# Optimization experiments

Measured on AMD Instinct MI355X. Metric: run time of the kernel, lower is better.

## Reference

```python
import jax, jax.numpy as jnp
import numpy as np

S = 4096  # source_sequence_size
Q = 4096  # query_sequence_size
E = 2048  # embedding_size
D = 2048  # output_embedding_size


def setup_inputs() -> dict:
    key = jax.random.key(0)
    ks = jax.random.split(key, 9)
    s = 1.0 / np.sqrt(E)
    return {
        "key": jax.random.normal(ks[0], (S, E), jnp.float32),
        "value": jax.random.normal(ks[1], (S, E), jnp.float32),
        "query": jax.random.normal(ks[2], (Q, E), jnp.float32),
        "Wk": jax.random.normal(ks[3], (D, E), jnp.float32) * s,
        "bk": jax.random.normal(ks[4], (D,), jnp.float32) * 0.01,
        "Wq": jax.random.normal(ks[5], (D, E), jnp.float32) * s,
        "bq": jax.random.normal(ks[6], (D,), jnp.float32) * 0.01,
        "Wv": jax.random.normal(ks[7], (D, E), jnp.float32) * s,
        "bv": jax.random.normal(ks[8], (D,), jnp.float32) * 0.01,
    }


def reference(key, value, query, Wk, bk, Wq, bq, Wv, bv):
    # Linear projections (nn.Linear: x @ W.T + b)
    k = key @ Wk.T + bk      # [S, D]
    v = value @ Wv.T + bv    # [S, D]
    q = query @ Wq.T + bq    # [Q, D]
    # Per-query-token attention scores over all source tokens (schema BOTH),
    # then weighted sum over value rows -- vectorized form of the per-token
    # apply_attention_scores loop.
    scale = 1.0 / jnp.sqrt(jnp.asarray(D, q.dtype))
    scores = jax.nn.softmax(jnp.einsum("qd,sd->qs", q, k) * scale, axis=-1)  # [Q, S]
    return jnp.einsum("qs,sd->qd", scores, v)  # [Q, D]
```

## Files before the change

kernel.cpp:

```cpp
#include <hip/hip_runtime.h>

#define S_SEQ 4096
#define Q_SEQ 4096
#define E_DIM 2048
#define D_DIM 2048

typedef __bf16 bf16;
typedef __bf16 bf16x4 __attribute__((ext_vector_type(4)));
typedef __bf16 bf16x8 __attribute__((ext_vector_type(8)));
typedef float f32x4 __attribute__((ext_vector_type(4)));

__global__ __launch_bounds__(256) void cast6(
    const float* __restrict__ i0, const float* __restrict__ i1,
    const float* __restrict__ i2, const float* __restrict__ i3,
    const float* __restrict__ i4, const float* __restrict__ i5,
    bf16* __restrict__ o0, bf16* __restrict__ o1, bf16* __restrict__ o2,
    bf16* __restrict__ o3, bf16* __restrict__ o4, bf16* __restrict__ o5) {
  const float* in;
  bf16* out;
  int n4;
  switch (blockIdx.y) {
    case 0: in = i0; out = o0; n4 = (S_SEQ * E_DIM) / 4; break;
    case 1: in = i1; out = o1; n4 = (S_SEQ * E_DIM) / 4; break;
    case 2: in = i2; out = o2; n4 = (S_SEQ * E_DIM) / 4; break;
    case 3: in = i3; out = o3; n4 = (D_DIM * E_DIM) / 4; break;
    case 4: in = i4; out = o4; n4 = (D_DIM * E_DIM) / 4; break;
    default: in = i5; out = o5; n4 = (D_DIM * E_DIM) / 4; break;
  }
  int i = blockIdx.x * 256 + threadIdx.x;
  if (i < n4) {
    float4 v = reinterpret_cast<const float4*>(in)[i];
    bf16x4 o;
    o[0] = (bf16)v.x; o[1] = (bf16)v.y; o[2] = (bf16)v.z; o[3] = (bf16)v.w;
    *reinterpret_cast<bf16x4*>(out + 4 * (size_t)i) = o;
  }
}

__device__ __forceinline__ void async_copy16(const bf16* g, bf16* l) {
  __builtin_amdgcn_global_load_lds(
      (const __attribute__((address_space(1))) void*)g,
      (__attribute__((address_space(3))) void*)l, 16, 0, 0);
}

__device__ __forceinline__ void xcd_remap32(int id, int nt, int& m, int& n) {
  int xcd = id & 7;
  int lid = id >> 3;
  m = (xcd & 3) * 8 + (lid & 7);
  n = (xcd >> 2) * (nt >> 1) + (lid >> 3);
}
__device__ __forceinline__ void xcd_remap16(int id, int nt, int& m, int& n) {
  int xcd = id & 7;
  int lid = id >> 3;
  m = (xcd & 3) * 4 + (lid & 3);
  n = (xcd >> 2) * (nt >> 1) + (lid >> 2);
}

template <int EPI>
__device__ __forceinline__ void gemm_body_sb(
    const bf16* __restrict__ A, int lda,
    const bf16* __restrict__ B, int ldb,
    void* __restrict__ C, int ldc,
    const float* __restrict__ aux, float scale, int K, int mBase, int nBase) {
  __shared__ __align__(16) bf16 Als[128 * 64];
  __shared__ __align__(16) bf16 Bls[128 * 64];

  const int tid  = threadIdx.x;
  const int wave = tid >> 6;
  const int lane = tid & 63;
  const int quad = lane >> 4;
  const int lrow = lane & 15;
  const int wRow = (wave >> 1) * 64;
  const int wCol = (wave & 1) * 64;

  f32x4 acc[4][4];
#pragma unroll
  for (int i = 0; i < 4; ++i)
#pragma unroll
    for (int j = 0; j < 4; ++j) {
      f32x4 z = {0.f, 0.f, 0.f, 0.f};
      acc[i][j] = z;
    }

  for (int k0 = 0; k0 < K; k0 += 64) {
#pragma unroll
    for (int c = 0; c < 4; ++c) {
      int chunk = c * 256 + tid;
      int row = chunk >> 3;
      int kc = (chunk & 7) ^ (row & 7);
      const bf16* g = A + (size_t)(mBase + row) * lda + k0 + kc * 8;
      async_copy16(g, Als + (size_t)(c * 256 + wave * 64) * 8);
    }
#pragma unroll
    for (int c = 0; c < 4; ++c) {
      int chunk = c * 256 + tid;
      int row = chunk >> 3;
      int kc = (chunk & 7) ^ (row & 7);
      const bf16* g = B + (size_t)(nBase + row) * ldb + k0 + kc * 8;
      async_copy16(g, Bls + (size_t)(c * 256 + wave * 64) * 8);
    }
    __syncthreads();

#pragma unroll
    for (int kk = 0; kk < 2; ++kk) {
      bf16x8 af[4], bfr[4];
#pragma unroll
      for (int i = 0; i < 4; ++i) {
        int r = wRow + i * 16 + lrow;
        int slot = (kk * 4 + quad) ^ (r & 7);
        af[i] = *(const bf16x8*)(Als + (size_t)r * 64 + slot * 8);
      }
#pragma unroll
      for (int j = 0; j < 4; ++j) {
        int r = wCol + j * 16 + lrow;
        int slot = (kk * 4 + quad) ^ (r & 7);
        bfr[j] = *(const bf16x8*)(Bls + (size_t)r * 64 + slot * 8);
      }
#pragma unroll
      for (int i = 0; i < 4; ++i)
#pragma unroll
        for (int j = 0; j < 4; ++j)
          acc[i][j] = __builtin_amdgcn_mfma_f32_16x16x32_bf16(af[i], bfr[j], acc[i][j], 0, 0, 0);
    }
    __syncthreads();
  }

  float rinv[4][4];
  if (EPI == 2) {
#pragma unroll
    for (int i = 0; i < 4; ++i)
#pragma unroll
      for (int r = 0; r < 4; ++r)
        rinv[i][r] = aux[mBase + wRow + i * 16 + quad * 4 + r];
  }
#pragma unroll
  for (int j = 0; j < 4; ++j) {
    const int cn = nBase + wCol + j * 16 + lrow;
    float bj = 0.f;
    if (EPI == 0) bj = aux[cn];
#pragma unroll
    for (int i = 0; i < 4; ++i) {
      const int rbase = mBase + wRow + i * 16 + quad * 4;
#pragma unroll
      for (int r = 0; r < 4; ++r) {
        if (EPI == 0)
          ((bf16*)C)[(size_t)(rbase + r) * ldc + cn] = (bf16)(acc[i][j][r] + bj);
        else if (EPI == 1)
          ((bf16*)C)[(size_t)(rbase + r) * ldc + cn] =
              (bf16)__expf(acc[i][j][r] * scale);
        else
          ((float*)C)[(size_t)(rbase + r) * ldc + cn] = acc[i][j][r] * rinv[i][r];
      }
    }
  }
}

__device__ __forceinline__ void stage_half(const bf16* __restrict__ G, int ld,
                                           int grow0, int k0, bf16* lds,
                                           int wave, int lane) {
#pragma unroll
  for (int s = 0; s < 2; ++s) {
    int c = (wave * 2 + s) * 64 + lane;
    int row = c >> 3;
    int kc = (c & 7) ^ (row & 7);
    const bf16* g = G + (size_t)(grow0 + row) * ld + k0 + kc * 8;
    async_copy16(g, lds + (size_t)(wave * 2 + s) * 512);
  }
}

#define BARRIER __builtin_amdgcn_s_barrier()
#define LGKM0 asm volatile("s_waitcnt lgkmcnt(0)" ::: "memory")
#define VMCNT2 asm volatile("s_waitcnt vmcnt(2)" ::: "memory")
#define VMCNT0 asm volatile("s_waitcnt vmcnt(0)" ::: "memory")

#define RD_A(buf, IP)                                                         \
  _Pragma("unroll") for (int ii = 0; ii < 2; ++ii)                            \
  _Pragma("unroll") for (int kk = 0; kk < 2; ++kk)                            \
      aR[ii][kk] = *(const bf16x8*)(&Als[buf][(size_t)(wRow + ((IP)*2 + ii) * 16 + lrow) * 64 + slotk[kk] * 8]);

#define RD_B(buf, JP, dst)                                                    \
  _Pragma("unroll") for (int jj = 0; jj < 2; ++jj)                            \
  _Pragma("unroll") for (int kk = 0; kk < 2; ++kk)                            \
      dst[jj][kk] = *(const bf16x8*)(&Bls[buf][(size_t)(wCol + ((JP)*2 + jj) * 16 + lrow) * 64 + slotk[kk] * 8]);

#define MMA16(IP)                                                              \
  __builtin_amdgcn_s_setprio(1);                                               \
  _Pragma("unroll") for (int jj = 0; jj < 2; ++jj)                             \
  _Pragma("unroll") for (int ii = 0; ii < 2; ++ii)                             \
  _Pragma("unroll") for (int kk = 0; kk < 2; ++kk)                             \
      acc[(IP)*2 + ii][jj] = __builtin_amdgcn_mfma_f32_16x16x32_bf16(          \
          aR[ii][kk], b0[jj][kk], acc[(IP)*2 + ii][jj], 0, 0, 0);              \
  _Pragma("unroll") for (int jj = 0; jj < 2; ++jj)                             \
  _Pragma("unroll") for (int ii = 0; ii < 2; ++ii)                             \
  _Pragma("unroll") for (int kk = 0; kk < 2; ++kk)                             \
      acc[(IP)*2 + ii][2 + jj] = __builtin_amdgcn_mfma_f32_16x16x32_bf16(      \
          aR[ii][kk], b1[jj][kk], acc[(IP)*2 + ii][2 + jj], 0, 0, 0);          \
  __builtin_amdgcn_s_setprio(0)

template <int EPI>
__device__ __forceinline__ void gemm_body_4ph(
    const bf16* __restrict__ A, int lda,
    const bf16* __restrict__ B, int ldb,
    void* __restrict__ C, int ldc,
    const float* __restrict__ aux, float scale, int K, int mBase, int nBase) {
  __shared__ __align__(16) bf16 Als[2][256 * 64];
  __shared__ __align__(16) bf16 Bls[2][128 * 64];

  const int tid  = threadIdx.x;
  const int wave = tid >> 6;
  const int lane = tid & 63;
  const int quad = lane >> 4;
  const int lrow = lane & 15;
  const int wRow = (wave >> 1) * 64;
  const int wCol = (wave & 1) * 64;
  const int slotk[2] = {quad ^ (lrow & 7), (4 + quad) ^ (lrow & 7)};

  f32x4 acc[4][4];
#pragma unroll
  for (int i = 0; i < 4; ++i)
#pragma unroll
    for (int j = 0; j < 4; ++j) {
      f32x4 z = {0.f, 0.f, 0.f, 0.f};
      acc[i][j] = z;
    }

  bf16x8 aR[2][2], b0[2][2], b1[2][2];

  stage_half(B, ldb, nBase, 0, &Bls[0][0], wave, lane);
  stage_half(A, lda, mBase, 0, &Als[0][0], wave, lane);
  stage_half(A, lda, mBase + 128, 0, &Als[0][128 * 64], wave, lane);
  stage_half(B, ldb, nBase, 64, &Bls[1][0], wave, lane);
  VMCNT2;
  BARRIER;

  const int NI = K >> 7;
#pragma unroll 1
  for (int i = 0; i < NI; ++i) {
    const bool nl = (i + 1 < NI);
    const int kb = i * 128;
    RD_A(0, 0);
    RD_B(0, 0, b0);
    RD_B(0, 1, b1);
    stage_half(A, lda, mBase, kb + 64, &Als[1][0], wave, lane);
    stage_half(A, lda, mBase + 128, kb + 64, &Als[1][128 * 64], wave, lane);
    BARRIER; LGKM0; MMA16(0); BARRIER;
    RD_A(0, 1);
    if (nl) {
      stage_half(B, ldb, nBase, kb + 128, &Bls[0][0], wave, lane);
      VMCNT2;
    } else {
      VMCNT0;
    }
    BARRIER; LGKM0; MMA16(1); BARRIER;
    RD_A(1, 0);
    RD_B(1, 0, b0);
    RD_B(1, 1, b1);
    if (nl) {
      stage_half(A, lda, mBase, kb + 128, &Als[0][0], wave, lane);
      stage_half(A, lda, mBase + 128, kb + 128, &Als[0][128 * 64], wave, lane);
    }
    BARRIER; LGKM0; MMA16(0); BARRIER;
    RD_A(1, 1);
    if (nl) {
      stage_half(B, ldb, nBase, kb + 192, &Bls[1][0], wave, lane);
      VMCNT2;
    }
    BARRIER; LGKM0; MMA16(1); BARRIER;
  }

  float rinv[4][4];
  if (EPI == 2) {
#pragma unroll
    for (int i = 0; i < 4; ++i)
#pragma unroll
      for (int r = 0; r < 4; ++r)
        rinv[i][r] = aux[mBase + wRow + i * 16 + quad * 4 + r];
  }
#pragma unroll
  for (int j = 0; j < 4; ++j) {
    const int cn = nBase + wCol + j * 16 + lrow;
    float bj = 0.f;
    if (EPI == 0) bj = aux[cn];
#pragma unroll
    for (int i = 0; i < 4; ++i) {
      const int rbase = mBase + wRow + i * 16 + quad * 4;
#pragma unroll
      for (int r = 0; r < 4; ++r) {
        if (EPI == 0)
          ((bf16*)C)[(size_t)(rbase + r) * ldc + cn] = (bf16)(acc[i][j][r] + bj);
        else if (EPI == 1)
          ((bf16*)C)[(size_t)(rbase + r) * ldc + cn] =
              (bf16)__expf(acc[i][j][r] * scale);
        else
          ((float*)C)[(size_t)(rbase + r) * ldc + cn] = acc[i][j][r] * rinv[i][r];
      }
    }
  }
}

__global__ __launch_bounds__(512, 2) void qk_gemm(
    const bf16* __restrict__ A, const bf16* __restrict__ B,
    bf16* __restrict__ E, float scale) {
  int m, n;
  xcd_remap16(blockIdx.x, 32, m, n);
  gemm_body_4ph<1>(A, D_DIM, B, D_DIM, (void*)E, S_SEQ, nullptr, scale, D_DIM,
                   m * 256, n * 128);
}

__global__ __launch_bounds__(512, 2) void pv_gemm(
    const bf16* __restrict__ E, const bf16* __restrict__ vT,
    float* __restrict__ out, const float* __restrict__ inv) {
  int m, n;
  xcd_remap16(blockIdx.x, 16, m, n);
  gemm_body_4ph<2>(E, S_SEQ, vT, S_SEQ, (void*)out, D_DIM, inv, 0.f, S_SEQ,
                   m * 256, n * 128);
}

__global__ __launch_bounds__(256, 2) void proj_gemm(
    const bf16* __restrict__ xk, const bf16* __restrict__ xq,
    const bf16* __restrict__ xv,
    const bf16* __restrict__ Wk, const bf16* __restrict__ Wq,
    const bf16* __restrict__ Wv,
    const float* __restrict__ bk, const float* __restrict__ bq,
    const float* __restrict__ bv,
    bf16* __restrict__ ok, bf16* __restrict__ oq, bf16* __restrict__ ov) {
  const bf16 *A, *W;
  const float* b;
  bf16* o;
  switch (blockIdx.z) {
    case 0: A = xk; W = Wk; b = bk; o = ok; break;
    case 1: A = xq; W = Wq; b = bq; o = oq; break;
    default: A = xv; W = Wv; b = bv; o = ov; break;
  }
  int m, n;
  xcd_remap32(blockIdx.x, 16, m, n);
  gemm_body_sb<0>(A, E_DIM, W, E_DIM, (void*)o, D_DIM, b, 0.f, E_DIM,
                  m * 128, n * 128);
}

__global__ __launch_bounds__(256) void transpose_bf16(
    const bf16* __restrict__ in, bf16* __restrict__ out) {
  __shared__ bf16 tile[64][66];
  const int t = threadIdx.x;
  const int c0 = blockIdx.x * 64;
  const int r0 = blockIdx.y * 64;
  const int col = t & 63;
  const int r4 = t >> 6;
#pragma unroll
  for (int i = 0; i < 16; ++i) {
    int rr = i * 4 + r4;
    tile[rr][col] = in[(size_t)(r0 + rr) * D_DIM + c0 + col];
  }
  __syncthreads();
#pragma unroll
  for (int i = 0; i < 16; ++i) {
    int rr = i * 4 + r4;
    out[(size_t)(c0 + rr) * S_SEQ + r0 + col] = tile[col][rr];
  }
}

__global__ __launch_bounds__(256) void rowsum_inv(
    const bf16* __restrict__ E, float* __restrict__ inv) {
  const int t = threadIdx.x;
  const int wave = t >> 6;
  const int lane = t & 63;
  const int row = blockIdx.x * 4 + wave;
  const bf16x8* src = (const bf16x8*)(E + (size_t)row * S_SEQ);
  float s = 0.f;
#pragma unroll
  for (int i = 0; i < 8; ++i) {
    bf16x8 v = src[lane + i * 64];
#pragma unroll
    for (int j = 0; j < 8; ++j) s += (float)v[j];
  }
#pragma unroll
  for (int off = 32; off > 0; off >>= 1)
    s += __shfl_down(s, off, 64);
  if (lane == 0) inv[row] = 1.0f / s;
}

extern "C" void kernel_launch(void* const* d_in, const int* in_sizes, int n_in,
                              void* d_out, int out_size, void* d_ws, size_t ws_size,
                              hipStream_t stream) {
  const float* key   = (const float*)d_in[0];
  const float* value = (const float*)d_in[1];
  const float* query = (const float*)d_in[2];
  const float* Wk = (const float*)d_in[3];
  const float* bk = (const float*)d_in[4];
  const float* Wq = (const float*)d_in[5];
  const float* bq = (const float*)d_in[6];
  const float* Wv = (const float*)d_in[7];
  const float* bv = (const float*)d_in[8];

  const size_t MB = 1ull << 20;
  char* ws = (char*)d_ws;
  bf16* key_bf   = (bf16*)(ws + 0 * MB);
  bf16* value_bf = (bf16*)(ws + 16 * MB);
  bf16* query_bf = (bf16*)(ws + 32 * MB);
  bf16* Wk_bf    = (bf16*)(ws + 48 * MB);
  bf16* Wq_bf    = (bf16*)(ws + 56 * MB);
  bf16* Wv_bf    = (bf16*)(ws + 64 * MB);
  bf16* k_bf     = (bf16*)(ws + 72 * MB);
  bf16* q_bf     = (bf16*)(ws + 88 * MB);
  bf16* v_bf     = (bf16*)(ws + 104 * MB);
  bf16* vT_bf    = (bf16*)(ws + 120 * MB);
  bf16* E        = (bf16*)(ws + 0 * MB);
  float* inv     = (float*)(ws + 34 * MB);

  dim3 blk(256);
  dim3 blk512(512);

  cast6<<<dim3(8192, 6), blk, 0, stream>>>(
      key, value, query, Wk, Wq, Wv,
      key_bf, value_bf, query_bf, Wk_bf, Wq_bf, Wv_bf);

  proj_gemm<<<dim3(512, 1, 3), blk, 0, stream>>>(
      key_bf, query_bf, value_bf, Wk_bf, Wq_bf, Wv_bf, bk, bq, bv,
      k_bf, q_bf, v_bf);

  transpose_bf16<<<dim3(D_DIM / 64, S_SEQ / 64), blk, 0, stream>>>(v_bf, vT_bf);

  const float scale = 0.022097086912079608f;
  qk_gemm<<<dim3(512), blk512, 0, stream>>>(q_bf, k_bf, E, scale);

  rowsum_inv<<<dim3(1024), blk, 0, stream>>>(E, inv);

  pv_gemm<<<dim3(256), blk512, 0, stream>>>(E, vT_bf, (float*)d_out, inv);
}
```

Before: 416.0 us.

## Fuse softmax row-sum into QK epilogue and fold V transpose into QK launch

The QK GEMM epilogue now sums the bf16 exponentials it writes, reduces them across lanes, and stores per-64-column partial row sums. A tiny kernel then adds 64 partials per row to get the inverse normaliser, replacing a pass that re-read the whole 4096x4096 score matrix. The V transpose moves into extra blocks appended to the QK grid, removing one launch and letting it overlap the GEMM. The cost is extra epilogue shuffles in the QK kernel, and transpose blocks that reserve the GEMM's shared-memory footprint.

```diff
diff --git a/kernel.cpp b/kernel.cpp
--- a/kernel.cpp
+++ b/kernel.cpp
@@ -201,7 +201,8 @@
     const bf16* __restrict__ A, int lda,
     const bf16* __restrict__ B, int ldb,
     void* __restrict__ C, int ldc,
-    const float* __restrict__ aux, float scale, int K, int mBase, int nBase) {
+    const float* __restrict__ aux, float scale, int K, int mBase, int nBase,
+    float* __restrict__ psum) {
   __shared__ __align__(16) bf16 Als[2][256 * 64];
   __shared__ __align__(16) bf16 Bls[2][128 * 64];
 
@@ -275,6 +276,13 @@
       for (int r = 0; r < 4; ++r)
         rinv[i][r] = aux[mBase + wRow + i * 16 + quad * 4 + r];
   }
+  float sp[4][4];
+  if (EPI == 1) {
+#pragma unroll
+    for (int i = 0; i < 4; ++i)
+#pragma unroll
+      for (int r = 0; r < 4; ++r) sp[i][r] = 0.f;
+  }
 #pragma unroll
   for (int j = 0; j < 4; ++j) {
     const int cn = nBase + wCol + j * 16 + lrow;
@@ -285,13 +293,35 @@
       const int rbase = mBase + wRow + i * 16 + quad * 4;
 #pragma unroll
       for (int r = 0; r < 4; ++r) {
-        if (EPI == 0)
+        if (EPI == 0) {
           ((bf16*)C)[(size_t)(rbase + r) * ldc + cn] = (bf16)(acc[i][j][r] + bj);
-        else if (EPI == 1)
-          ((bf16*)C)[(size_t)(rbase + r) * ldc + cn] =
-              (bf16)__expf(acc[i][j][r] * scale);
-        else
+        } else if (EPI == 1) {
+          bf16 eb = (bf16)__expf(acc[i][j][r] * scale);
+          ((bf16*)C)[(size_t)(rbase + r) * ldc + cn] = eb;
+          sp[i][r] += (float)eb;
+        } else {
           ((float*)C)[(size_t)(rbase + r) * ldc + cn] = acc[i][j][r] * rinv[i][r];
+        }
+      }
+    }
+  }
+  if (EPI == 1) {
+#pragma unroll
+    for (int i = 0; i < 4; ++i)
+#pragma unroll
+      for (int r = 0; r < 4; ++r) {
+#pragma unroll
+        for (int off = 1; off < 16; off <<= 1)
+          sp[i][r] += __shfl_xor(sp[i][r], off, 64);
+      }
+    if (lrow == 0) {
+      const int col64 = (nBase + wCol) >> 6;
+#pragma unroll
+      for (int i = 0; i < 4; ++i) {
+        const int rbase = mBase + wRow + i * 16 + quad * 4;
+#pragma unroll
+        for (int r = 0; r < 4; ++r)
+          psum[(size_t)(rbase + r) * 64 + col64] = sp[i][r];
       }
     }
   }
@@ -299,11 +329,39 @@
 
 __global__ __launch_bounds__(512, 2) void qk_gemm(
     const bf16* __restrict__ A, const bf16* __restrict__ B,
-    bf16* __restrict__ E, float scale) {
+    bf16* __restrict__ E, float scale,
+    const bf16* __restrict__ v, bf16* __restrict__ vT,
+    float* __restrict__ psum) {
+  if (blockIdx.x >= 512) {
+    __shared__ bf16 ttile[64][66];
+    const int t = threadIdx.x;
+    const int col = t & 63;
+    const int r8 = t >> 6;
+    const int base = (blockIdx.x - 512) * 4;
+#pragma unroll 1
+    for (int t4 = 0; t4 < 4; ++t4) {
+      const int id = base + t4;
+      const int c0 = (id & 31) * 64;
+      const int r0 = (id >> 5) * 64;
+#pragma unroll
+      for (int i = 0; i < 8; ++i) {
+        int rr = i * 8 + r8;
+        ttile[rr][col] = v[(size_t)(r0 + rr) * D_DIM + c0 + col];
+      }
+      __syncthreads();
+#pragma unroll
+      for (int i = 0; i < 8; ++i) {
+        int rr = i * 8 + r8;
+        vT[(size_t)(c0 + rr) * S_SEQ + r0 + col] = ttile[col][rr];
+      }
+      __syncthreads();
+    }
+    return;
+  }
   int m, n;
   xcd_remap16(blockIdx.x, 32, m, n);
   gemm_body_4ph<1>(A, D_DIM, B, D_DIM, (void*)E, S_SEQ, nullptr, scale, D_DIM,
-                   m * 256, n * 128);
+                   m * 256, n * 128, psum);
 }
 
 __global__ __launch_bounds__(512, 2) void pv_gemm(
@@ -312,7 +370,7 @@
   int m, n;
   xcd_remap16(blockIdx.x, 16, m, n);
   gemm_body_4ph<2>(E, S_SEQ, vT, S_SEQ, (void*)out, D_DIM, inv, 0.f, S_SEQ,
-                   m * 256, n * 128);
+                   m * 256, n * 128, nullptr);
 }
 
 __global__ __launch_bounds__(256, 2) void proj_gemm(
@@ -337,45 +395,17 @@
                   m * 128, n * 128);
 }
 
-__global__ __launch_bounds__(256) void transpose_bf16(
-    const bf16* __restrict__ in, bf16* __restrict__ out) {
-  __shared__ bf16 tile[64][66];
-  const int t = threadIdx.x;
-  const int c0 = blockIdx.x * 64;
-  const int r0 = blockIdx.y * 64;
-  const int col = t & 63;
-  const int r4 = t >> 6;
+__global__ __launch_bounds__(256) void rowsum2(
+    const float* __restrict__ psum, float* __restrict__ inv) {
+  const int r = blockIdx.x * 256 + threadIdx.x;
+  const f32x4* p = (const f32x4*)(psum + (size_t)r * 64);
+  float s = 0.f;
 #pragma unroll
   for (int i = 0; i < 16; ++i) {
-    int rr = i * 4 + r4;
-    tile[rr][col] = in[(size_t)(r0 + rr) * D_DIM + c0 + col];
-  }
-  __syncthreads();
-#pragma unroll
-  for (int i = 0; i < 16; ++i) {
-    int rr = i * 4 + r4;
-    out[(size_t)(c0 + rr) * S_SEQ + r0 + col] = tile[col][rr];
-  }
-}
-
-__global__ __launch_bounds__(256) void rowsum_inv(
-    const bf16* __restrict__ E, float* __restrict__ inv) {
-  const int t = threadIdx.x;
-  const int wave = t >> 6;
-  const int lane = t & 63;
-  const int row = blockIdx.x * 4 + wave;
-  const bf16x8* src = (const bf16x8*)(E + (size_t)row * S_SEQ);
-  float s = 0.f;
-#pragma unroll
-  for (int i = 0; i < 8; ++i) {
-    bf16x8 v = src[lane + i * 64];
-#pragma unroll
-    for (int j = 0; j < 8; ++j) s += (float)v[j];
-  }
-#pragma unroll
-  for (int off = 32; off > 0; off >>= 1)
-    s += __shfl_down(s, off, 64);
-  if (lane == 0) inv[row] = 1.0f / s;
+    f32x4 v = p[i];
+    s += v[0] + v[1] + v[2] + v[3];
+  }
+  inv[r] = 1.0f / s;
 }
 
 extern "C" void kernel_launch(void* const* d_in, const int* in_sizes, int n_in,
@@ -404,7 +434,8 @@
   bf16* v_bf     = (bf16*)(ws + 104 * MB);
   bf16* vT_bf    = (bf16*)(ws + 120 * MB);
   bf16* E        = (bf16*)(ws + 0 * MB);
-  float* inv     = (float*)(ws + 34 * MB);
+  float* psum    = (float*)(ws + 34 * MB);
+  float* inv     = (float*)(ws + 35 * MB);
 
   dim3 blk(256);
   dim3 blk512(512);
@@ -417,12 +448,11 @@
       key_bf, query_bf, value_bf, Wk_bf, Wq_bf, Wv_bf, bk, bq, bv,
       k_bf, q_bf, v_bf);
 
-  transpose_bf16<<<dim3(D_DIM / 64, S_SEQ / 64), blk, 0, stream>>>(v_bf, vT_bf);
-
   const float scale = 0.022097086912079608f;
-  qk_gemm<<<dim3(512), blk512, 0, stream>>>(q_bf, k_bf, E, scale);
-
-  rowsum_inv<<<dim3(1024), blk, 0, stream>>>(E, inv);
+  qk_gemm<<<dim3(1024), blk512, 0, stream>>>(q_bf, k_bf, E, scale,
+                                             v_bf, vT_bf, psum);
+
+  rowsum2<<<dim3(16), blk, 0, stream>>>(psum, inv);
 
   pv_gemm<<<dim3(256), blk512, 0, stream>>>(E, vT_bf, (float*)d_out, inv);
 }
```

Result: no change. 419.3 us (+0.8%).
